# Performance work log

Hardware: AMD Instinct MI355X
Metric: run time of the kernel (lower is better)

## Reference

```python
import jax, jax.numpy as jnp
import numpy as np

N_POINTS = 1048576
LEVELS = 16
LOG2T = 19
TABLE_SIZE = 1 << LOG2T  # 524288
FEAT = 2
MIN_RES = 16.0
MAX_RES = 512.0


def setup_inputs() -> dict:
    key = jax.random.key(0)
    kx, kt = jax.random.split(key)
    bounding_box = jnp.array([[-1.5, -1.5, -1.5], [1.5, 1.5, 1.5]], dtype=jnp.float32)
    # sample mostly inside the box, a few points slightly outside to exercise clamp/keep_mask
    x = jax.random.uniform(kx, (N_POINTS, 3), dtype=jnp.float32, minval=-1.6, maxval=1.6)
    # torch init: uniform(-1e-4, 1e-4) per level embedding table
    tables = jax.random.uniform(kt, (LEVELS, TABLE_SIZE, FEAT), dtype=jnp.float32,
                                minval=-1e-4, maxval=1e-4)
    return {"x": x, "bounding_box": bounding_box, "tables": tables}


def _hash_encode(x, bounding_box, tables):
    min_b, max_b = bounding_box[0], bounding_box[1]  # [3]
    # keep_mask: point unchanged by clamping in every dim
    keep_mask = jnp.all((x >= min_b) & (x <= max_b), axis=-1)
    xc = jnp.clip(x, min_b, max_b)
    u = (xc - min_b) / (max_b - min_b)  # normalized to [0,1], [N,3]

    b = jnp.exp((jnp.log(MAX_RES) - jnp.log(MIN_RES)) / (LEVELS - 1))
    PI = jnp.array([1, 2654435761, 805459861], dtype=jnp.uint32)
    HASH_MASK = jnp.uint32(TABLE_SIZE - 1)
    # 8 corner offsets in (i,j,k) order matching the torch module
    offs = jnp.array([[i, j, k] for i in (0, 1) for j in (0, 1) for k in (0, 1)],
                     dtype=jnp.int32)  # [8,3]

    outs = []
    for level in range(LEVELS):
        Nl = jnp.floor(MIN_RES * b ** level)            # scalar resolution
        box_size = (max_b - min_b) / Nl                 # [3]
        grid = jnp.floor(u * Nl).astype(jnp.int32)      # [N,3] min-corner grid coords
        vmin = grid.astype(x.dtype) * box_size + min_b  # [N,3]
        vmax = vmin + box_size                          # [N,3]
        corners = (grid[:, None, :] + offs[None, :, :]).astype(jnp.uint32)  # [N,8,3]
        # spatial hash: xor of coord*prime, wrap-around in uint32 matches low bits of torch int64
        h = (corners[..., 0] * PI[0]) ^ (corners[..., 1] * PI[1]) ^ (corners[..., 2] * PI[2])
        idx = (h & HASH_MASK).astype(jnp.int32)         # [N,8]
        emb = tables[level][idx]                        # gather -> [N,8,F]
        # trilinear interpolation; note: uses ORIGINAL (unclamped) x, as in the torch code
        w = (x - vmin) / (vmax - vmin)                  # [N,3]
        wx, wy, wz = w[:, 0:1], w[:, 1:2], w[:, 2:3]
        c00 = emb[:, 0] * (1 - wx) + emb[:, 4] * wx
        c01 = emb[:, 1] * (1 - wx) + emb[:, 5] * wx
        c10 = emb[:, 2] * (1 - wx) + emb[:, 6] * wx
        c11 = emb[:, 3] * (1 - wx) + emb[:, 7] * wx
        c0 = c00 * (1 - wy) + c10 * wy
        c1 = c01 * (1 - wy) + c11 * wy
        outs.append(c0 * (1 - wz) + c1 * wz)            # [N,F]
    return jnp.concatenate(outs, axis=-1), keep_mask    # [N, L*F], [N]


def reference(x, bounding_box, tables):
    return _hash_encode(x, bounding_box, tables)
```

## Files before the change

### kernel.cpp

```cpp
#include <hip/hip_runtime.h>

#define NPTS   1048576
#define NLEV   16
#define TSIZE  (1u << 19)
#define HMASK  (TSIZE - 1u)
#define NBUCK  32768

__device__ __constant__ float NLF_TAB[16] = {
    16.f, 20.f, 25.f, 32.f, 40.f, 50.f, 64.f, 80.f,
    101.f, 128.f, 161.f, 203.f, 256.f, 322.f, 406.f, 512.f};

__device__ __forceinline__ unsigned spread5(unsigned x) {
    x &= 0x1F;
    x = (x | (x << 8)) & 0x100F;
    x = (x | (x << 4)) & 0x10C3;
    x = (x | (x << 2)) & 0x1249;
    return x;
}

__device__ __forceinline__ unsigned morton_key(float u0, float u1, float u2) {
    unsigned k0 = min(31u, (unsigned)(u0 * 32.0f));
    unsigned k1 = min(31u, (unsigned)(u1 * 32.0f));
    unsigned k2 = min(31u, (unsigned)(u2 * 32.0f));
    return (spread5(k0) << 2) | (spread5(k1) << 1) | spread5(k2);
}

__device__ __forceinline__ void uvw(float x0, float x1, float x2,
                                    float* u0, float* u1, float* u2) {
    const float mn = -1.5f, mx = 1.5f, rng = 3.0f;
    *u0 = (fminf(fmaxf(x0, mn), mx) - mn) / rng;
    *u1 = (fminf(fmaxf(x1, mn), mx) - mn) / rng;
    *u2 = (fminf(fmaxf(x2, mn), mx) - mn) / rng;
}

__device__ __forceinline__ void level_lerp(
    float x0, float x1, float x2, float u0, float u1, float u2,
    float Nl, const float2* __restrict__ tab, float* r0, float* r1)
{
#pragma clang fp contract(off)
    const float mn = -1.5f, rng = 3.0f;
    const float box = rng / Nl;

    int g0 = (int)floorf(u0 * Nl);
    int g1 = (int)floorf(u1 * Nl);
    int g2 = (int)floorf(u2 * Nl);

    float vmin0 = (float)g0 * box + mn;
    float vmin1 = (float)g1 * box + mn;
    float vmin2 = (float)g2 * box + mn;

    float den0 = (vmin0 + box) - vmin0;
    float den1 = (vmin1 + box) - vmin1;
    float den2 = (vmin2 + box) - vmin2;

    float wx = (x0 - vmin0) / den0;
    float wy = (x1 - vmin1) / den1;
    float wz = (x2 - vmin2) / den2;

    unsigned hx0 = (unsigned)g0;
    unsigned hx1 = (unsigned)(g0 + 1);
    unsigned hy0 = (unsigned)g1       * 2654435761u;
    unsigned hy1 = (unsigned)(g1 + 1) * 2654435761u;
    unsigned hz0 = (unsigned)g2       * 805459861u;
    unsigned hz1 = (unsigned)(g2 + 1) * 805459861u;

    float2 e000 = tab[(hx0 ^ hy0 ^ hz0) & HMASK];
    float2 e001 = tab[(hx0 ^ hy0 ^ hz1) & HMASK];
    float2 e010 = tab[(hx0 ^ hy1 ^ hz0) & HMASK];
    float2 e011 = tab[(hx0 ^ hy1 ^ hz1) & HMASK];
    float2 e100 = tab[(hx1 ^ hy0 ^ hz0) & HMASK];
    float2 e101 = tab[(hx1 ^ hy0 ^ hz1) & HMASK];
    float2 e110 = tab[(hx1 ^ hy1 ^ hz0) & HMASK];
    float2 e111 = tab[(hx1 ^ hy1 ^ hz1) & HMASK];

    float omx = 1.0f - wx, omy = 1.0f - wy, omz = 1.0f - wz;
    {
        float c00 = e000.x * omx + e100.x * wx;
        float c01 = e001.x * omx + e101.x * wx;
        float c10 = e010.x * omx + e110.x * wx;
        float c11 = e011.x * omx + e111.x * wx;
        float c0  = c00 * omy + c10 * wy;
        float c1  = c01 * omy + c11 * wy;
        *r0 = c0 * omz + c1 * wz;
    }
    {
        float c00 = e000.y * omx + e100.y * wx;
        float c01 = e001.y * omx + e101.y * wx;
        float c10 = e010.y * omx + e110.y * wx;
        float c11 = e011.y * omx + e111.y * wx;
        float c0  = c00 * omy + c10 * wy;
        float c1  = c01 * omy + c11 * wy;
        *r1 = c0 * omz + c1 * wz;
    }
}


__global__ __launch_bounds__(256)
void hist_kernel(const float* __restrict__ xin, unsigned* __restrict__ hist)
{
    int p = blockIdx.x * 256 + threadIdx.x;
    if (p >= NPTS) return;
    float x0 = xin[3 * p], x1 = xin[3 * p + 1], x2 = xin[3 * p + 2];
    float u0, u1, u2; uvw(x0, x1, x2, &u0, &u1, &u2);
    atomicAdd(&hist[morton_key(u0, u1, u2)], 1u);
}

__global__ __launch_bounds__(1024)
void scan_kernel(unsigned* __restrict__ hist, unsigned* __restrict__ cursor)
{
    __shared__ unsigned part[1024];
    int t = threadIdx.x;
    unsigned local[32];
    unsigned s = 0;
#pragma unroll
    for (int i = 0; i < 32; ++i) { local[i] = hist[t * 32 + i]; s += local[i]; }
    part[t] = s;
    __syncthreads();
    for (int off = 1; off < 1024; off <<= 1) {
        unsigned v = (t >= off) ? part[t - off] : 0;
        __syncthreads();
        part[t] += v;
        __syncthreads();
    }
    unsigned base = (t == 0) ? 0u : part[t - 1];
#pragma unroll
    for (int i = 0; i < 32; ++i) {
        cursor[t * 32 + i] = base;
        base += local[i];
    }
}

__global__ __launch_bounds__(256)
void scatter_kernel(const float* __restrict__ xin,
                    unsigned* __restrict__ cursor,
                    unsigned* __restrict__ sidx,
                    float4* __restrict__ sx4)
{
    int p = blockIdx.x * 256 + threadIdx.x;
    if (p >= NPTS) return;
    float x0 = xin[3 * p], x1 = xin[3 * p + 1], x2 = xin[3 * p + 2];
    float u0, u1, u2; uvw(x0, x1, x2, &u0, &u1, &u2);
    unsigned pos = atomicAdd(&cursor[morton_key(u0, u1, u2)], 1u);
    sidx[pos] = (unsigned)p;
    sx4[pos] = make_float4(x0, x1, x2, 0.0f);
}


__global__ __launch_bounds__(256)
void coarse_sorted(const unsigned* __restrict__ sidx,
                   const float4* __restrict__ sx4,
                   const float* __restrict__ tables,
                   float* __restrict__ out)
{
#pragma clang fp contract(off)
    int s = blockIdx.x * 256 + threadIdx.x;
    if (s >= NPTS) return;
    unsigned p = sidx[s];
    float4 xv = sx4[s];
    float u0, u1, u2; uvw(xv.x, xv.y, xv.z, &u0, &u1, &u2);

    float res[16];
#pragma unroll
    for (int l = 0; l < 8; ++l) {
        const float2* tab = (const float2*)tables + (size_t)l * TSIZE;
        level_lerp(xv.x, xv.y, xv.z, u0, u1, u2, NLF_TAB[l], tab,
                   &res[2 * l], &res[2 * l + 1]);
    }

    float4* orow = (float4*)(out + (size_t)p * 32);
#pragma unroll
    for (int i = 0; i < 4; ++i)
        orow[i] = make_float4(res[4 * i + 0], res[4 * i + 1],
                              res[4 * i + 2], res[4 * i + 3]);
}

template<int L, bool WRITE_MASK>
__global__ __launch_bounds__(256)
void fine_kernel(const float* __restrict__ xin,
                 const float* __restrict__ tables,
                 float* __restrict__ out)
{
#pragma clang fp contract(off)
    int p = blockIdx.x * 256 + threadIdx.x;
    if (p >= NPTS) return;
    float x0 = xin[3 * p], x1 = xin[3 * p + 1], x2 = xin[3 * p + 2];
    float u0, u1, u2; uvw(x0, x1, x2, &u0, &u1, &u2);

    const float2* tab = (const float2*)tables + (size_t)L * TSIZE;
    float r0, r1;
    level_lerp(x0, x1, x2, u0, u1, u2, NLF_TAB[L], tab, &r0, &r1);
    *(float2*)(out + (size_t)p * 32 + 2 * L) = make_float2(r0, r1);

    if (WRITE_MASK) {
        const float mn = -1.5f, mx = 1.5f;
        float keep = (x0 >= mn && x0 <= mx &&
                      x1 >= mn && x1 <= mx &&
                      x2 >= mn && x2 <= mx) ? 1.0f : 0.0f;
        out[(size_t)NPTS * 32 + p] = keep;
    }
}


__global__ __launch_bounds__(256)
void coarse_kernel(const float* __restrict__ xin,
                   const float* __restrict__ tables,
                   float* __restrict__ out)
{
#pragma clang fp contract(off)
    int p = blockIdx.x * 256 + threadIdx.x;
    if (p >= NPTS) return;
    float x0 = xin[3 * p], x1 = xin[3 * p + 1], x2 = xin[3 * p + 2];
    float u0, u1, u2; uvw(x0, x1, x2, &u0, &u1, &u2);

    float res[16];
#pragma unroll
    for (int l = 0; l < 8; ++l) {
        const float2* tab = (const float2*)tables + (size_t)l * TSIZE;
        level_lerp(x0, x1, x2, u0, u1, u2, NLF_TAB[l], tab,
                   &res[2 * l], &res[2 * l + 1]);
    }
    float4* orow = (float4*)(out + (size_t)p * 32);
#pragma unroll
    for (int i = 0; i < 4; ++i)
        orow[i] = make_float4(res[4 * i + 0], res[4 * i + 1],
                              res[4 * i + 2], res[4 * i + 3]);
}

extern "C" void kernel_launch(void* const* d_in, const int* in_sizes, int n_in,
                              void* d_out, int out_size, void* d_ws, size_t ws_size,
                              hipStream_t stream) {
    const float* x      = (const float*)d_in[0];
    const float* tables = (const float*)d_in[2];
    float* out = (float*)d_out;

    int n = in_sizes[0] / 3;
    int blocks = (n + 255) / 256;

    const size_t HIST_B   = (size_t)NBUCK * 4;
    const size_t SIDX_OFF = 131072;
    const size_t SX4_OFF  = SIDX_OFF + (size_t)NPTS * 4;
    const size_t NEEDED   = SX4_OFF + (size_t)NPTS * 16;

    if (ws_size >= NEEDED) {
        unsigned* hist = (unsigned*)d_ws;
        unsigned* sidx = (unsigned*)((char*)d_ws + SIDX_OFF);
        float4*   sx4  = (float4*)((char*)d_ws + SX4_OFF);

        hipMemsetAsync(hist, 0, HIST_B, stream);
        hist_kernel<<<blocks, 256, 0, stream>>>(x, hist);
        scan_kernel<<<1, 1024, 0, stream>>>(hist, hist);
        scatter_kernel<<<blocks, 256, 0, stream>>>(x, hist, sidx, sx4);

        coarse_sorted<<<blocks, 256, 0, stream>>>(sidx, sx4, tables, out);
    } else {
        coarse_kernel<<<blocks, 256, 0, stream>>>(x, tables, out);
    }

    fine_kernel< 8, false><<<blocks, 256, 0, stream>>>(x, tables, out);
    fine_kernel< 9, false><<<blocks, 256, 0, stream>>>(x, tables, out);
    fine_kernel<10, true ><<<blocks, 256, 0, stream>>>(x, tables, out);
    fine_kernel<11, false><<<blocks, 256, 0, stream>>>(x, tables, out);
    fine_kernel<12, false><<<blocks, 256, 0, stream>>>(x, tables, out);
    fine_kernel<13, false><<<blocks, 256, 0, stream>>>(x, tables, out);
    fine_kernel<14, false><<<blocks, 256, 0, stream>>>(x, tables, out);
    fine_kernel<15, false><<<blocks, 256, 0, stream>>>(x, tables, out);
}
```

Before: 525.8 us.

## Fuse histogram into first fine-level kernel and extend sorted coarse pass to ten levels

```diff
diff --git a/kernel.cpp b/kernel.cpp
--- a/kernel.cpp
+++ b/kernel.cpp
@@ -95,16 +95,6 @@
 }
 
 
-__global__ __launch_bounds__(256)
-void hist_kernel(const float* __restrict__ xin, unsigned* __restrict__ hist)
-{
-    int p = blockIdx.x * 256 + threadIdx.x;
-    if (p >= NPTS) return;
-    float x0 = xin[3 * p], x1 = xin[3 * p + 1], x2 = xin[3 * p + 2];
-    float u0, u1, u2; uvw(x0, x1, x2, &u0, &u1, &u2);
-    atomicAdd(&hist[morton_key(u0, u1, u2)], 1u);
-}
-
 __global__ __launch_bounds__(1024)
 void scan_kernel(unsigned* __restrict__ hist, unsigned* __restrict__ cursor)
 {
@@ -147,10 +137,10 @@
 
 
 __global__ __launch_bounds__(256)
-void coarse_sorted(const unsigned* __restrict__ sidx,
-                   const float4* __restrict__ sx4,
-                   const float* __restrict__ tables,
-                   float* __restrict__ out)
+void coarse10_sorted(const unsigned* __restrict__ sidx,
+                     const float4* __restrict__ sx4,
+                     const float* __restrict__ tables,
+                     float* __restrict__ out)
 {
 #pragma clang fp contract(off)
     int s = blockIdx.x * 256 + threadIdx.x;
@@ -159,9 +149,9 @@
     float4 xv = sx4[s];
     float u0, u1, u2; uvw(xv.x, xv.y, xv.z, &u0, &u1, &u2);
 
-    float res[16];
-#pragma unroll
-    for (int l = 0; l < 8; ++l) {
+    float res[20];
+#pragma unroll
+    for (int l = 0; l < 10; ++l) {
         const float2* tab = (const float2*)tables + (size_t)l * TSIZE;
         level_lerp(xv.x, xv.y, xv.z, u0, u1, u2, NLF_TAB[l], tab,
                    &res[2 * l], &res[2 * l + 1]);
@@ -169,22 +159,26 @@
 
     float4* orow = (float4*)(out + (size_t)p * 32);
 #pragma unroll
-    for (int i = 0; i < 4; ++i)
+    for (int i = 0; i < 5; ++i)
         orow[i] = make_float4(res[4 * i + 0], res[4 * i + 1],
                               res[4 * i + 2], res[4 * i + 3]);
 }
 
-template<int L, bool WRITE_MASK>
+template<int L, bool WRITE_MASK, bool FUSE_HIST>
 __global__ __launch_bounds__(256)
 void fine_kernel(const float* __restrict__ xin,
                  const float* __restrict__ tables,
-                 float* __restrict__ out)
-{
-#pragma clang fp contract(off)
-    int p = blockIdx.x * 256 + threadIdx.x;
-    if (p >= NPTS) return;
-    float x0 = xin[3 * p], x1 = xin[3 * p + 1], x2 = xin[3 * p + 2];
-    float u0, u1, u2; uvw(x0, x1, x2, &u0, &u1, &u2);
+                 float* __restrict__ out,
+                 unsigned* __restrict__ hist)
+{
+#pragma clang fp contract(off)
+    int p = blockIdx.x * 256 + threadIdx.x;
+    if (p >= NPTS) return;
+    float x0 = xin[3 * p], x1 = xin[3 * p + 1], x2 = xin[3 * p + 2];
+    float u0, u1, u2; uvw(x0, x1, x2, &u0, &u1, &u2);
+
+    if (FUSE_HIST)
+        atomicAdd(&hist[morton_key(u0, u1, u2)], 1u);
 
     const float2* tab = (const float2*)tables + (size_t)L * TSIZE;
     float r0, r1;
@@ -226,6 +220,24 @@
                               res[4 * i + 2], res[4 * i + 3]);
 }
 
+template<int L>
+__global__ __launch_bounds__(256)
+void fine_plain(const float* __restrict__ xin,
+                const float* __restrict__ tables,
+                float* __restrict__ out)
+{
+#pragma clang fp contract(off)
+    int p = blockIdx.x * 256 + threadIdx.x;
+    if (p >= NPTS) return;
+    float x0 = xin[3 * p], x1 = xin[3 * p + 1], x2 = xin[3 * p + 2];
+    float u0, u1, u2; uvw(x0, x1, x2, &u0, &u1, &u2);
+
+    const float2* tab = (const float2*)tables + (size_t)L * TSIZE;
+    float r0, r1;
+    level_lerp(x0, x1, x2, u0, u1, u2, NLF_TAB[L], tab, &r0, &r1);
+    *(float2*)(out + (size_t)p * 32 + 2 * L) = make_float2(r0, r1);
+}
+
 extern "C" void kernel_launch(void* const* d_in, const int* in_sizes, int n_in,
                               void* d_out, int out_size, void* d_ws, size_t ws_size,
                               hipStream_t stream) {
@@ -247,21 +259,26 @@
         float4*   sx4  = (float4*)((char*)d_ws + SX4_OFF);
 
         hipMemsetAsync(hist, 0, HIST_B, stream);
-        hist_kernel<<<blocks, 256, 0, stream>>>(x, hist);
+
+        fine_kernel<15, false, true ><<<blocks, 256, 0, stream>>>(x, tables, out, hist);
+        fine_kernel<14, false, false><<<blocks, 256, 0, stream>>>(x, tables, out, hist);
+        fine_kernel<13, false, false><<<blocks, 256, 0, stream>>>(x, tables, out, hist);
+        fine_kernel<12, false, false><<<blocks, 256, 0, stream>>>(x, tables, out, hist);
+        fine_kernel<11, false, false><<<blocks, 256, 0, stream>>>(x, tables, out, hist);
+        fine_kernel<10, true , false><<<blocks, 256, 0, stream>>>(x, tables, out, hist);
+
         scan_kernel<<<1, 1024, 0, stream>>>(hist, hist);
         scatter_kernel<<<blocks, 256, 0, stream>>>(x, hist, sidx, sx4);
-
-        coarse_sorted<<<blocks, 256, 0, stream>>>(sidx, sx4, tables, out);
+        coarse10_sorted<<<blocks, 256, 0, stream>>>(sidx, sx4, tables, out);
     } else {
         coarse_kernel<<<blocks, 256, 0, stream>>>(x, tables, out);
-    }
-
-    fine_kernel< 8, false><<<blocks, 256, 0, stream>>>(x, tables, out);
-    fine_kernel< 9, false><<<blocks, 256, 0, stream>>>(x, tables, out);
-    fine_kernel<10, true ><<<blocks, 256, 0, stream>>>(x, tables, out);
-    fine_kernel<11, false><<<blocks, 256, 0, stream>>>(x, tables, out);
-    fine_kernel<12, false><<<blocks, 256, 0, stream>>>(x, tables, out);
-    fine_kernel<13, false><<<blocks, 256, 0, stream>>>(x, tables, out);
-    fine_kernel<14, false><<<blocks, 256, 0, stream>>>(x, tables, out);
-    fine_kernel<15, false><<<blocks, 256, 0, stream>>>(x, tables, out);
-}
+        fine_plain< 8><<<blocks, 256, 0, stream>>>(x, tables, out);
+        fine_plain< 9><<<blocks, 256, 0, stream>>>(x, tables, out);
+        fine_kernel<10, true , false><<<blocks, 256, 0, stream>>>(x, tables, out, nullptr);
+        fine_plain<11><<<blocks, 256, 0, stream>>>(x, tables, out);
+        fine_plain<12><<<blocks, 256, 0, stream>>>(x, tables, out);
+        fine_plain<13><<<blocks, 256, 0, stream>>>(x, tables, out);
+        fine_plain<14><<<blocks, 256, 0, stream>>>(x, tables, out);
+        fine_plain<15><<<blocks, 256, 0, stream>>>(x, tables, out);
+    }
+}
```

After: 444.7 us. 15.4% less time.
